# Performance work log

Hardware: AMD Instinct MI355X
Metric: run time of the kernel (lower is better)

Reference implementation:

```python
import jax, jax.numpy as jnp
import numpy as np

B, NQ, NKV = 8, 2048, 2048
DQ, DKV, H = 1024, 1024, 256


def setup_inputs() -> dict:
    key = jax.random.key(0)
    ks = jax.random.split(key, 12)
    s = 0.02
    return {
        "x_q": jax.random.normal(ks[0], (B, NQ, DQ), jnp.float32),
        "x_kv": jax.random.normal(ks[1], (B, NKV, DKV), jnp.float32),
        "bias": jax.random.normal(ks[2], (B, NQ, NKV), jnp.float32),
        "wq_w": jax.random.normal(ks[3], (DQ, H), jnp.float32) * s,
        "wq_b": jnp.zeros((H,), jnp.float32),
        "wk_w": jax.random.normal(ks[4], (DKV, H), jnp.float32) * s,
        "wk_b": jnp.zeros((H,), jnp.float32),
        "wv_w": jax.random.normal(ks[5], (DKV, H), jnp.float32) * s,
        "wv_b": jnp.zeros((H,), jnp.float32),
        "f2_w": jax.random.normal(ks[6], (H, H), jnp.float32) * s,
        "f2_b": jnp.zeros((H,), jnp.float32),
    }


def reference(x_q, x_kv, bias, wq_w, wq_b, wk_w, wk_b, wv_w, wv_b, f2_w, f2_b):
    # Projections: [B, nq, H], [B, nkv, H]
    Q = jnp.einsum('bsd,dh->bsh', x_q, wq_w) + wq_b
    K = jnp.einsum('btd,dh->bth', x_kv, wk_w) + wk_b
    V = jnp.einsum('btd,dh->bth', x_kv, wv_w) + wv_b
    exp_w = jnp.exp(bias)          # [B, nq, nkv]
    exp_K = jnp.exp(K)             # [B, nkv, H]
    num = jnp.einsum('bst,bth->bsh', exp_w, exp_K * V)
    den = jnp.einsum('bst,bth->bsh', exp_w, exp_K)
    Yt = jax.nn.sigmoid(Q) * (num / den)
    return jnp.einsum('bsh,hg->bsg', Yt, f2_w) + f2_b
```

## Files before the change

kernel.cpp:

```cpp
#include <hip/hip_runtime.h>
#include <cstddef>
#include <cstdint>

#define BATCH 8
#define NQ    2048
#define NKV   2048
#define DIN   1024
#define HD    256

typedef __attribute__((ext_vector_type(8))) short bf16x8;
typedef __attribute__((ext_vector_type(4))) float f32x4;

__device__ __forceinline__ float sigmoidf_(float x) {
    return 1.0f / (1.0f + expf(-x));
}

__device__ __forceinline__ unsigned short f2bf(float f) {
    union { float f; unsigned int u; } v;
    v.f = f;
    unsigned int u = v.u;
    return (unsigned short)((u + 0x7FFFu + ((u >> 16) & 1u)) >> 16);
}

#define GLL16(gp, lp)                                                        \
    __builtin_amdgcn_global_load_lds(                                        \
        (const __attribute__((address_space(1))) void*)(gp),                 \
        (__attribute__((address_space(3))) void*)(lp), 16, 0, 0)

__global__ __launch_bounds__(256)
void wtrans_kernel(const float* __restrict__ w0, const float* __restrict__ w1,
                   const float* __restrict__ w2,
                   unsigned short* __restrict__ t0, unsigned short* __restrict__ t1,
                   unsigned short* __restrict__ t2)
{
    const float* w = (blockIdx.z == 0) ? w0 : (blockIdx.z == 1) ? w1 : w2;
    unsigned short* t = (blockIdx.z == 0) ? t0 : (blockIdx.z == 1) ? t1 : t2;
    const int k0 = blockIdx.y * 64;
    const int n0 = blockIdx.x * 64;
    const int tid = threadIdx.x;
    const int kq = tid >> 4;
    const int nq = tid & 15;
    float4 r[4];
#pragma unroll
    for (int i = 0; i < 4; ++i)
        r[i] = *(const float4*)&w[(size_t)(k0 + kq * 4 + i) * HD + n0 + nq * 4];
#pragma unroll
    for (int j = 0; j < 4; ++j) {
        ushort4 o;
        o.x = f2bf(((const float*)&r[0])[j]);
        o.y = f2bf(((const float*)&r[1])[j]);
        o.z = f2bf(((const float*)&r[2])[j]);
        o.w = f2bf(((const float*)&r[3])[j]);
        *(ushort4*)&t[(size_t)(n0 + nq * 4 + j) * DIN + k0 + kq * 4] = o;
    }
}

#define TS 64
#define TH 256
#define TK 32
#define A_LD 40

__global__ __launch_bounds__(256, 1)
void proj_q_mfma(const float* __restrict__ X,
                 const unsigned short* __restrict__ WT,
                 const float* __restrict__ bv,
                 float* __restrict__ sigQ)
{
    __shared__ unsigned short As[2][TS][A_LD];
    __shared__ unsigned short Bs[2][TH * TK];

    const int m0 = blockIdx.x * TS;
    const int tid = threadIdx.x;
    const int lane = tid & 63, wave = tid >> 6;
    const int quad = lane >> 4, l16 = lane & 15;

    const int a_row = tid >> 2, a_koff = (tid & 3) * 8;
    const float* aP = X + (size_t)(m0 + a_row) * DIN + a_koff;

    const unsigned short* bP[4];
    int ldsOff[4];
#pragma unroll
    for (int j = 0; j < 4; ++j) {
        int idx = j * 256 + tid;
        int row = idx >> 2, c = idx & 3;
        int kc = c ^ ((row >> 1) & 3);
        bP[j] = WT + (size_t)row * DIN + kc * 8;
        ldsOff[j] = (j * 256 + wave * 64) * 16;
    }

    f32x4 acc[4][4] = {};
    float4 a0 = *(const float4*)aP;
    float4 a1 = *(const float4*)(aP + 4);

    for (int k0 = 0; k0 < DIN; k0 += TK) {
        const int p = (k0 >> 5) & 1;
        ushort4 q0, q1;
        q0.x = f2bf(a0.x); q0.y = f2bf(a0.y); q0.z = f2bf(a0.z); q0.w = f2bf(a0.w);
        q1.x = f2bf(a1.x); q1.y = f2bf(a1.y); q1.z = f2bf(a1.z); q1.w = f2bf(a1.w);
        *(ushort4*)&As[p][a_row][a_koff]     = q0;
        *(ushort4*)&As[p][a_row][a_koff + 4] = q1;
        char* bL = (char*)&Bs[p][0];
#pragma unroll
        for (int j = 0; j < 4; ++j)
            GLL16(bP[j] + k0, bL + ldsOff[j]);
        __syncthreads();
        if (k0 + TK < DIN) {
            a0 = *(const float4*)(aP + k0 + TK);
            a1 = *(const float4*)(aP + k0 + TK + 4);
        }
        bf16x8 af[4], bf[4];
#pragma unroll
        for (int rt = 0; rt < 4; ++rt)
            af[rt] = *(const bf16x8*)&As[p][rt * 16 + l16][quad * 8];
#pragma unroll
        for (int ct = 0; ct < 4; ++ct) {
            int row = wave * 64 + ct * 16 + l16;
            int off = row * 64 + ((quad ^ ((row >> 1) & 3)) * 16);
            bf[ct] = *(const bf16x8*)((const char*)&Bs[p][0] + off);
        }
#pragma unroll
        for (int rt = 0; rt < 4; ++rt)
#pragma unroll
            for (int ct = 0; ct < 4; ++ct)
                acc[rt][ct] = __builtin_amdgcn_mfma_f32_16x16x32_bf16(
                    af[rt], bf[ct], acc[rt][ct], 0, 0, 0);
        __syncthreads();
    }

#pragma unroll
    for (int rt = 0; rt < 4; ++rt)
#pragma unroll
        for (int ct = 0; ct < 4; ++ct) {
            const int h = wave * 64 + ct * 16 + l16;
            const float bb = bv[h];
#pragma unroll
            for (int r = 0; r < 4; ++r) {
                const int m = m0 + rt * 16 + quad * 4 + r;
                sigQ[(size_t)m * HD + h] = sigmoidf_(acc[rt][ct][r] + bb);
            }
        }
}

__global__ __launch_bounds__(256, 1)
void proj_kv_mfma(const float* __restrict__ X,
                  const unsigned short* __restrict__ WKT,
                  const float* __restrict__ bk,
                  const unsigned short* __restrict__ WVT,
                  const float* __restrict__ bvv,
                  unsigned short* __restrict__ eKt,
                  unsigned short* __restrict__ eKVt)
{
    __shared__ unsigned short As[2][TS][A_LD];
    __shared__ unsigned short Bk[2][TH * TK];
    __shared__ unsigned short Bv[2][TH * TK];

    const int m0 = blockIdx.x * TS;
    const int tid = threadIdx.x;
    const int lane = tid & 63, wave = tid >> 6;
    const int quad = lane >> 4, l16 = lane & 15;

    const int a_row = tid >> 2, a_koff = (tid & 3) * 8;
    const float* aP = X + (size_t)(m0 + a_row) * DIN + a_koff;

    const unsigned short* bkP[4];
    const unsigned short* bvP[4];
    int ldsOff[4];
#pragma unroll
    for (int j = 0; j < 4; ++j) {
        int idx = j * 256 + tid;
        int row = idx >> 2, c = idx & 3;
        int kc = c ^ ((row >> 1) & 3);
        bkP[j] = WKT + (size_t)row * DIN + kc * 8;
        bvP[j] = WVT + (size_t)row * DIN + kc * 8;
        ldsOff[j] = (j * 256 + wave * 64) * 16;
    }

    f32x4 acck[4][4] = {};
    f32x4 accv[4][4] = {};
    float4 a0 = *(const float4*)aP;
    float4 a1 = *(const float4*)(aP + 4);

    for (int k0 = 0; k0 < DIN; k0 += TK) {
        const int p = (k0 >> 5) & 1;
        ushort4 q0, q1;
        q0.x = f2bf(a0.x); q0.y = f2bf(a0.y); q0.z = f2bf(a0.z); q0.w = f2bf(a0.w);
        q1.x = f2bf(a1.x); q1.y = f2bf(a1.y); q1.z = f2bf(a1.z); q1.w = f2bf(a1.w);
        *(ushort4*)&As[p][a_row][a_koff]     = q0;
        *(ushort4*)&As[p][a_row][a_koff + 4] = q1;
        char* bkL = (char*)&Bk[p][0];
        char* bvL = (char*)&Bv[p][0];
#pragma unroll
        for (int j = 0; j < 4; ++j) {
            GLL16(bkP[j] + k0, bkL + ldsOff[j]);
            GLL16(bvP[j] + k0, bvL + ldsOff[j]);
        }
        __syncthreads();
        if (k0 + TK < DIN) {
            a0 = *(const float4*)(aP + k0 + TK);
            a1 = *(const float4*)(aP + k0 + TK + 4);
        }
        bf16x8 af[4], bkf[4], bvf[4];
#pragma unroll
        for (int rt = 0; rt < 4; ++rt)
            af[rt] = *(const bf16x8*)&As[p][rt * 16 + l16][quad * 8];
#pragma unroll
        for (int ct = 0; ct < 4; ++ct) {
            int row = wave * 64 + ct * 16 + l16;
            int off = row * 64 + ((quad ^ ((row >> 1) & 3)) * 16);
            bkf[ct] = *(const bf16x8*)((const char*)&Bk[p][0] + off);
            bvf[ct] = *(const bf16x8*)((const char*)&Bv[p][0] + off);
        }
#pragma unroll
        for (int rt = 0; rt < 4; ++rt)
#pragma unroll
            for (int ct = 0; ct < 4; ++ct) {
                acck[rt][ct] = __builtin_amdgcn_mfma_f32_16x16x32_bf16(
                    af[rt], bkf[ct], acck[rt][ct], 0, 0, 0);
                accv[rt][ct] = __builtin_amdgcn_mfma_f32_16x16x32_bf16(
                    af[rt], bvf[ct], accv[rt][ct], 0, 0, 0);
            }
        __syncthreads();
    }

    const int bidx = m0 >> 11;
    const int tb = m0 & (NKV - 1);
#pragma unroll
    for (int rt = 0; rt < 4; ++rt)
#pragma unroll
        for (int ct = 0; ct < 4; ++ct) {
            const int h = wave * 64 + ct * 16 + l16;
            const float bkb = bk[h];
            const float bvb = bvv[h];
            ushort4 pk, pv;
            unsigned short* pK = (unsigned short*)&pk;
            unsigned short* pV = (unsigned short*)&pv;
#pragma unroll
            for (int r = 0; r < 4; ++r) {
                float e  = __expf(acck[rt][ct][r] + bkb);
                float ev = e * (accv[rt][ct][r] + bvb);
                pK[r] = f2bf(e);
                pV[r] = f2bf(ev);
            }
            const int t0 = tb + rt * 16 + quad * 4;
            size_t base = ((size_t)bidx * HD + h) * NKV + t0;
            *(ushort4*)&eKt[base]  = pk;
            *(ushort4*)&eKVt[base] = pv;
        }
}

__global__ __launch_bounds__(256, 1)
void aft_mfma_kernel(const float* __restrict__ bias,
                     const unsigned short* __restrict__ eKt,
                     const unsigned short* __restrict__ eKVt,
                     const float* __restrict__ sigQ,
                     float* __restrict__ Yt)
{
    __shared__ unsigned short As[2][TS][A_LD];
    __shared__ unsigned short Bn[2][TH * TK];
    __shared__ unsigned short Bd[2][TH * TK];

    const int b  = blockIdx.y;
    const int s0 = blockIdx.x * TS;
    const int tid = threadIdx.x;
    const int lane = tid & 63, wave = tid >> 6;
    const int quad = lane >> 4, l16 = lane & 15;

    const int a_row = tid >> 2, a_koff = (tid & 3) * 8;
    const float* aP = bias + ((size_t)b * NQ + (s0 + a_row)) * NKV + a_koff;

    const unsigned short* bnP[4];
    const unsigned short* bdP[4];
    int ldsOff[4];
#pragma unroll
    for (int j = 0; j < 4; ++j) {
        int idx = j * 256 + tid;
        int row = idx >> 2, c = idx & 3;
        int kc = c ^ ((row >> 1) & 3);
        bnP[j] = eKVt + ((size_t)b * HD + row) * NKV + kc * 8;
        bdP[j] = eKt  + ((size_t)b * HD + row) * NKV + kc * 8;
        ldsOff[j] = (j * 256 + wave * 64) * 16;
    }

    f32x4 accn[4][4] = {};
    f32x4 accd[4][4] = {};
    float4 a0 = *(const float4*)aP;
    float4 a1 = *(const float4*)(aP + 4);

    for (int k0 = 0; k0 < NKV; k0 += TK) {
        const int p = (k0 >> 5) & 1;
        ushort4 q0, q1;
        q0.x = f2bf(__expf(a0.x)); q0.y = f2bf(__expf(a0.y));
        q0.z = f2bf(__expf(a0.z)); q0.w = f2bf(__expf(a0.w));
        q1.x = f2bf(__expf(a1.x)); q1.y = f2bf(__expf(a1.y));
        q1.z = f2bf(__expf(a1.z)); q1.w = f2bf(__expf(a1.w));
        *(ushort4*)&As[p][a_row][a_koff]     = q0;
        *(ushort4*)&As[p][a_row][a_koff + 4] = q1;
        char* bnL = (char*)&Bn[p][0];
        char* bdL = (char*)&Bd[p][0];
#pragma unroll
        for (int j = 0; j < 4; ++j) {
            GLL16(bnP[j] + k0, bnL + ldsOff[j]);
            GLL16(bdP[j] + k0, bdL + ldsOff[j]);
        }
        __syncthreads();
        if (k0 + TK < NKV) {
            a0 = *(const float4*)(aP + k0 + TK);
            a1 = *(const float4*)(aP + k0 + TK + 4);
        }
        bf16x8 af[4], bnf[4], bdf[4];
#pragma unroll
        for (int rt = 0; rt < 4; ++rt)
            af[rt] = *(const bf16x8*)&As[p][rt * 16 + l16][quad * 8];
#pragma unroll
        for (int ct = 0; ct < 4; ++ct) {
            int row = wave * 64 + ct * 16 + l16;
            int off = row * 64 + ((quad ^ ((row >> 1) & 3)) * 16);
            bnf[ct] = *(const bf16x8*)((const char*)&Bn[p][0] + off);
            bdf[ct] = *(const bf16x8*)((const char*)&Bd[p][0] + off);
        }
#pragma unroll
        for (int rt = 0; rt < 4; ++rt)
#pragma unroll
            for (int ct = 0; ct < 4; ++ct) {
                accn[rt][ct] = __builtin_amdgcn_mfma_f32_16x16x32_bf16(
                    af[rt], bnf[ct], accn[rt][ct], 0, 0, 0);
                accd[rt][ct] = __builtin_amdgcn_mfma_f32_16x16x32_bf16(
                    af[rt], bdf[ct], accd[rt][ct], 0, 0, 0);
            }
        __syncthreads();
    }

#pragma unroll
    for (int rt = 0; rt < 4; ++rt)
#pragma unroll
        for (int ct = 0; ct < 4; ++ct) {
            const int h = wave * 64 + ct * 16 + l16;
#pragma unroll
            for (int r = 0; r < 4; ++r) {
                const int s = s0 + rt * 16 + quad * 4 + r;
                const size_t idx = ((size_t)b * NQ + s) * HD + h;
                Yt[idx] = sigQ[idx] * accn[rt][ct][r] / accd[rt][ct][r];
            }
        }
}

#define BM 64
#define BN 64
#define BK 16
#define PADF 4
#define LDAF (BM + PADF)
#define LDBF (BN + PADF)

__global__ __launch_bounds__(256)
void gemm_bias_kernel(const float* __restrict__ X, const float* __restrict__ W,
                      const float* __restrict__ bv, float* __restrict__ out,
                      int M, int N, int K)
{
    __shared__ float As[BK][LDAF];
    __shared__ float Ws[BK][LDBF];
    const int tid = threadIdx.x;
    const int tx = tid & 15, ty = tid >> 4;
    const int row0 = blockIdx.y * BM;
    const int col0 = blockIdx.x * BN;
    const int la_row = tid >> 2, la_col = (tid & 3) * 4;
    const int lw_row = tid >> 4, lw_col = (tid & 15) * 4;

    float acc[4][4] = {};

    const float* Xp = X + (size_t)(row0 + la_row) * K + la_col;
    const float* Wp = W + (size_t)lw_row * N + col0 + lw_col;

    for (int k0 = 0; k0 < K; k0 += BK) {
        float4 av = *(const float4*)(Xp + k0);
        float4 wv = *(const float4*)(Wp + (size_t)k0 * N);
        As[la_col + 0][la_row] = av.x;
        As[la_col + 1][la_row] = av.y;
        As[la_col + 2][la_row] = av.z;
        As[la_col + 3][la_row] = av.w;
        *(float4*)&Ws[lw_row][lw_col] = wv;
        __syncthreads();
#pragma unroll
        for (int kk = 0; kk < BK; ++kk) {
            float4 a4 = *(const float4*)&As[kk][ty * 4];
            float4 w4 = *(const float4*)&Ws[kk][tx * 4];
            float aa[4] = {a4.x, a4.y, a4.z, a4.w};
            float ww[4] = {w4.x, w4.y, w4.z, w4.w};
#pragma unroll
            for (int i = 0; i < 4; ++i)
#pragma unroll
                for (int j = 0; j < 4; ++j)
                    acc[i][j] = fmaf(aa[i], ww[j], acc[i][j]);
        }
        __syncthreads();
    }

    float bb[4];
#pragma unroll
    for (int j = 0; j < 4; ++j) bb[j] = bv[col0 + tx * 4 + j];
#pragma unroll
    for (int i = 0; i < 4; ++i) {
        int r = row0 + ty * 4 + i;
        float4 o;
        o.x = acc[i][0] + bb[0];
        o.y = acc[i][1] + bb[1];
        o.z = acc[i][2] + bb[2];
        o.w = acc[i][3] + bb[3];
        *(float4*)&out[(size_t)r * N + col0 + tx * 4] = o;
    }
}

extern "C" void kernel_launch(void* const* d_in, const int* in_sizes, int n_in,
                              void* d_out, int out_size, void* d_ws, size_t ws_size,
                              hipStream_t stream)
{
    const float* x_q  = (const float*)d_in[0];
    const float* x_kv = (const float*)d_in[1];
    const float* bias = (const float*)d_in[2];
    const float* wq_w = (const float*)d_in[3];
    const float* wq_b = (const float*)d_in[4];
    const float* wk_w = (const float*)d_in[5];
    const float* wk_b = (const float*)d_in[6];
    const float* wv_w = (const float*)d_in[7];
    const float* wv_b = (const float*)d_in[8];
    const float* f2_w = (const float*)d_in[9];
    const float* f2_b = (const float*)d_in[10];
    float* out = (float*)d_out;

    float* ws = (float*)d_ws;
    const size_t nBH = (size_t)BATCH * NQ * HD;
    float* sigQ = ws;
    float* Yt   = ws + nBH;
    unsigned short* eKt  = (unsigned short*)(ws + 2 * nBH);
    unsigned short* eKVt = eKt + nBH;
    unsigned short* wqT  = eKVt + nBH;
    unsigned short* wkT  = wqT + (size_t)HD * DIN;
    unsigned short* wvT  = wkT + (size_t)HD * DIN;

    const int M = BATCH * NQ;
    dim3 blk(256);

    wtrans_kernel<<<dim3(HD / 64, DIN / 64, 3), blk, 0, stream>>>(
        wq_w, wk_w, wv_w, wqT, wkT, wvT);

    proj_q_mfma<<<dim3(M / TS), blk, 0, stream>>>(x_q, wqT, wq_b, sigQ);

    proj_kv_mfma<<<dim3(M / TS), blk, 0, stream>>>(
        x_kv, wkT, wk_b, wvT, wv_b, eKt, eKVt);

    aft_mfma_kernel<<<dim3(NQ / TS, BATCH), blk, 0, stream>>>(
        bias, eKt, eKVt, sigQ, Yt);

    gemm_bias_kernel<<<dim3(HD / BN, M / BM), blk, 0, stream>>>(
        Yt, f2_w, f2_b, out, M, HD, HD);
}
```

Baseline: 429.5 us.

## Halve row tile to 32 and allow two blocks per CU in MFMA kernels

Shrinks the row tile from 64 to 32 rows in the Q, KV and AFT MFMA kernels, remaps the A-tile load so each thread loads one float4, and raises launch bounds to two blocks per CU. The AFT kernel also interleaves batches in its block index so neighbouring blocks share the same query tile position across batches. The aim is more waves per CU and more blocks to fill the GPU, which can hide latency. The cost is that the K/V weight tiles are reloaded twice as often per output row and each block does fewer MFMAs per barrier.

```diff
diff --git a/kernel.cpp b/kernel.cpp
--- a/kernel.cpp
+++ b/kernel.cpp
@@ -55,12 +55,12 @@
     }
 }
 
-#define TS 64
+#define TS 32
 #define TH 256
 #define TK 32
 #define A_LD 40
 
-__global__ __launch_bounds__(256, 1)
+__global__ __launch_bounds__(256, 2)
 void proj_q_mfma(const float* __restrict__ X,
                  const unsigned short* __restrict__ WT,
                  const float* __restrict__ bv,
@@ -74,7 +74,7 @@
     const int lane = tid & 63, wave = tid >> 6;
     const int quad = lane >> 4, l16 = lane & 15;
 
-    const int a_row = tid >> 2, a_koff = (tid & 3) * 8;
+    const int a_row = tid >> 3, a_koff = (tid & 7) * 4;
     const float* aP = X + (size_t)(m0 + a_row) * DIN + a_koff;
 
     const unsigned short* bP[4];
@@ -88,29 +88,24 @@
         ldsOff[j] = (j * 256 + wave * 64) * 16;
     }
 
-    f32x4 acc[4][4] = {};
+    f32x4 acc[2][4] = {};
     float4 a0 = *(const float4*)aP;
-    float4 a1 = *(const float4*)(aP + 4);
 
     for (int k0 = 0; k0 < DIN; k0 += TK) {
         const int p = (k0 >> 5) & 1;
-        ushort4 q0, q1;
+        ushort4 q0;
         q0.x = f2bf(a0.x); q0.y = f2bf(a0.y); q0.z = f2bf(a0.z); q0.w = f2bf(a0.w);
-        q1.x = f2bf(a1.x); q1.y = f2bf(a1.y); q1.z = f2bf(a1.z); q1.w = f2bf(a1.w);
-        *(ushort4*)&As[p][a_row][a_koff]     = q0;
-        *(ushort4*)&As[p][a_row][a_koff + 4] = q1;
+        *(ushort4*)&As[p][a_row][a_koff] = q0;
         char* bL = (char*)&Bs[p][0];
 #pragma unroll
         for (int j = 0; j < 4; ++j)
             GLL16(bP[j] + k0, bL + ldsOff[j]);
         __syncthreads();
-        if (k0 + TK < DIN) {
+        if (k0 + TK < DIN)
             a0 = *(const float4*)(aP + k0 + TK);
-            a1 = *(const float4*)(aP + k0 + TK + 4);
-        }
-        bf16x8 af[4], bf[4];
-#pragma unroll
-        for (int rt = 0; rt < 4; ++rt)
+        bf16x8 af[2], bf[4];
+#pragma unroll
+        for (int rt = 0; rt < 2; ++rt)
             af[rt] = *(const bf16x8*)&As[p][rt * 16 + l16][quad * 8];
 #pragma unroll
         for (int ct = 0; ct < 4; ++ct) {
@@ -119,7 +114,7 @@
             bf[ct] = *(const bf16x8*)((const char*)&Bs[p][0] + off);
         }
 #pragma unroll
-        for (int rt = 0; rt < 4; ++rt)
+        for (int rt = 0; rt < 2; ++rt)
 #pragma unroll
             for (int ct = 0; ct < 4; ++ct)
                 acc[rt][ct] = __builtin_amdgcn_mfma_f32_16x16x32_bf16(
@@ -128,7 +123,7 @@
     }
 
 #pragma unroll
-    for (int rt = 0; rt < 4; ++rt)
+    for (int rt = 0; rt < 2; ++rt)
 #pragma unroll
         for (int ct = 0; ct < 4; ++ct) {
             const int h = wave * 64 + ct * 16 + l16;
@@ -141,7 +136,7 @@
         }
 }
 
-__global__ __launch_bounds__(256, 1)
+__global__ __launch_bounds__(256, 2)
 void proj_kv_mfma(const float* __restrict__ X,
                   const unsigned short* __restrict__ WKT,
                   const float* __restrict__ bk,
@@ -159,7 +154,7 @@
     const int lane = tid & 63, wave = tid >> 6;
     const int quad = lane >> 4, l16 = lane & 15;
 
-    const int a_row = tid >> 2, a_koff = (tid & 3) * 8;
+    const int a_row = tid >> 3, a_koff = (tid & 7) * 4;
     const float* aP = X + (size_t)(m0 + a_row) * DIN + a_koff;
 
     const unsigned short* bkP[4];
@@ -175,18 +170,15 @@
         ldsOff[j] = (j * 256 + wave * 64) * 16;
     }
 
-    f32x4 acck[4][4] = {};
-    f32x4 accv[4][4] = {};
+    f32x4 acck[2][4] = {};
+    f32x4 accv[2][4] = {};
     float4 a0 = *(const float4*)aP;
-    float4 a1 = *(const float4*)(aP + 4);
 
     for (int k0 = 0; k0 < DIN; k0 += TK) {
         const int p = (k0 >> 5) & 1;
-        ushort4 q0, q1;
+        ushort4 q0;
         q0.x = f2bf(a0.x); q0.y = f2bf(a0.y); q0.z = f2bf(a0.z); q0.w = f2bf(a0.w);
-        q1.x = f2bf(a1.x); q1.y = f2bf(a1.y); q1.z = f2bf(a1.z); q1.w = f2bf(a1.w);
-        *(ushort4*)&As[p][a_row][a_koff]     = q0;
-        *(ushort4*)&As[p][a_row][a_koff + 4] = q1;
+        *(ushort4*)&As[p][a_row][a_koff] = q0;
         char* bkL = (char*)&Bk[p][0];
         char* bvL = (char*)&Bv[p][0];
 #pragma unroll
@@ -195,13 +187,11 @@
             GLL16(bvP[j] + k0, bvL + ldsOff[j]);
         }
         __syncthreads();
-        if (k0 + TK < DIN) {
+        if (k0 + TK < DIN)
             a0 = *(const float4*)(aP + k0 + TK);
-            a1 = *(const float4*)(aP + k0 + TK + 4);
-        }
-        bf16x8 af[4], bkf[4], bvf[4];
-#pragma unroll
-        for (int rt = 0; rt < 4; ++rt)
+        bf16x8 af[2], bkf[4], bvf[4];
+#pragma unroll
+        for (int rt = 0; rt < 2; ++rt)
             af[rt] = *(const bf16x8*)&As[p][rt * 16 + l16][quad * 8];
 #pragma unroll
         for (int ct = 0; ct < 4; ++ct) {
@@ -211,7 +201,7 @@
             bvf[ct] = *(const bf16x8*)((const char*)&Bv[p][0] + off);
         }
 #pragma unroll
-        for (int rt = 0; rt < 4; ++rt)
+        for (int rt = 0; rt < 2; ++rt)
 #pragma unroll
             for (int ct = 0; ct < 4; ++ct) {
                 acck[rt][ct] = __builtin_amdgcn_mfma_f32_16x16x32_bf16(
@@ -225,7 +215,7 @@
     const int bidx = m0 >> 11;
     const int tb = m0 & (NKV - 1);
 #pragma unroll
-    for (int rt = 0; rt < 4; ++rt)
+    for (int rt = 0; rt < 2; ++rt)
 #pragma unroll
         for (int ct = 0; ct < 4; ++ct) {
             const int h = wave * 64 + ct * 16 + l16;
@@ -248,7 +238,7 @@
         }
 }
 
-__global__ __launch_bounds__(256, 1)
+__global__ __launch_bounds__(256, 2)
 void aft_mfma_kernel(const float* __restrict__ bias,
                      const unsigned short* __restrict__ eKt,
                      const unsigned short* __restrict__ eKVt,
@@ -259,13 +249,14 @@
     __shared__ unsigned short Bn[2][TH * TK];
     __shared__ unsigned short Bd[2][TH * TK];
 
-    const int b  = blockIdx.y;
-    const int s0 = blockIdx.x * TS;
+    const int lin = blockIdx.y * gridDim.x + blockIdx.x;
+    const int b   = lin & 7;
+    const int s0  = (lin >> 3) * TS;
     const int tid = threadIdx.x;
     const int lane = tid & 63, wave = tid >> 6;
     const int quad = lane >> 4, l16 = lane & 15;
 
-    const int a_row = tid >> 2, a_koff = (tid & 3) * 8;
+    const int a_row = tid >> 3, a_koff = (tid & 7) * 4;
     const float* aP = bias + ((size_t)b * NQ + (s0 + a_row)) * NKV + a_koff;
 
     const unsigned short* bnP[4];
@@ -281,20 +272,16 @@
         ldsOff[j] = (j * 256 + wave * 64) * 16;
     }
 
-    f32x4 accn[4][4] = {};
-    f32x4 accd[4][4] = {};
+    f32x4 accn[2][4] = {};
+    f32x4 accd[2][4] = {};
     float4 a0 = *(const float4*)aP;
-    float4 a1 = *(const float4*)(aP + 4);
 
     for (int k0 = 0; k0 < NKV; k0 += TK) {
         const int p = (k0 >> 5) & 1;
-        ushort4 q0, q1;
+        ushort4 q0;
         q0.x = f2bf(__expf(a0.x)); q0.y = f2bf(__expf(a0.y));
         q0.z = f2bf(__expf(a0.z)); q0.w = f2bf(__expf(a0.w));
-        q1.x = f2bf(__expf(a1.x)); q1.y = f2bf(__expf(a1.y));
-        q1.z = f2bf(__expf(a1.z)); q1.w = f2bf(__expf(a1.w));
-        *(ushort4*)&As[p][a_row][a_koff]     = q0;
-        *(ushort4*)&As[p][a_row][a_koff + 4] = q1;
+        *(ushort4*)&As[p][a_row][a_koff] = q0;
         char* bnL = (char*)&Bn[p][0];
         char* bdL = (char*)&Bd[p][0];
 #pragma unroll
@@ -303,13 +290,11 @@
             GLL16(bdP[j] + k0, bdL + ldsOff[j]);
         }
         __syncthreads();
-        if (k0 + TK < NKV) {
+        if (k0 + TK < NKV)
             a0 = *(const float4*)(aP + k0 + TK);
-            a1 = *(const float4*)(aP + k0 + TK + 4);
-        }
-        bf16x8 af[4], bnf[4], bdf[4];
-#pragma unroll
-        for (int rt = 0; rt < 4; ++rt)
+        bf16x8 af[2], bnf[4], bdf[4];
+#pragma unroll
+        for (int rt = 0; rt < 2; ++rt)
             af[rt] = *(const bf16x8*)&As[p][rt * 16 + l16][quad * 8];
 #pragma unroll
         for (int ct = 0; ct < 4; ++ct) {
@@ -319,7 +304,7 @@
             bdf[ct] = *(const bf16x8*)((const char*)&Bd[p][0] + off);
         }
 #pragma unroll
-        for (int rt = 0; rt < 4; ++rt)
+        for (int rt = 0; rt < 2; ++rt)
 #pragma unroll
             for (int ct = 0; ct < 4; ++ct) {
                 accn[rt][ct] = __builtin_amdgcn_mfma_f32_16x16x32_bf16(
@@ -331,7 +316,7 @@
     }
 
 #pragma unroll
-    for (int rt = 0; rt < 4; ++rt)
+    for (int rt = 0; rt < 2; ++rt)
 #pragma unroll
         for (int ct = 0; ct < 4; ++ct) {
             const int h = wave * 64 + ct * 16 + l16;
```

Measured after the change: 463.3 us. 1.08x slower.

## Software-pipeline MFMA GEMM loops with prefetch and manual waitcnt barriers

Applied to the files above, without the earlier changes.

The three MFMA GEMM kernels now issue the LDS-direct loads for the next B tile, and the fp32 A-operand loads two steps ahead, before the current tile is computed. Explicit s_waitcnt and s_barrier replace __syncthreads so that global memory latency overlaps with MFMA work. The attention-like kernel also remaps block indices so consecutive blocks cycle through batches, and the fp32 output GEMM gains register prefetch of the next tile. The manual vmcnt counts depend on the exact order in which loads are issued. Redundant loads at the tail are clamped to a valid address, adding some extra traffic.

```diff
diff --git a/kernel.cpp b/kernel.cpp
--- a/kernel.cpp
+++ b/kernel.cpp
@@ -26,6 +26,13 @@
     __builtin_amdgcn_global_load_lds(                                        \
         (const __attribute__((address_space(1))) void*)(gp),                 \
         (__attribute__((address_space(3))) void*)(lp), 16, 0, 0)
+
+__device__ __forceinline__ f32x4 gload4(const float* p) {
+    f32x4 r;
+    asm volatile("global_load_dwordx4 %0, %1, off"
+                 : "=v"(r) : "v"(p) : "memory");
+    return r;
+}
 
 __global__ __launch_bounds__(256)
 void wtrans_kernel(const float* __restrict__ w0, const float* __restrict__ w1,
@@ -89,25 +96,32 @@
     }
 
     f32x4 acc[4][4] = {};
-    float4 a0 = *(const float4*)aP;
-    float4 a1 = *(const float4*)(aP + 4);
+
+#pragma unroll
+    for (int j = 0; j < 4; ++j)
+        GLL16(bP[j], (char*)&Bs[0][0] + ldsOff[j]);
+    f32x4 c0 = gload4(aP);
+    f32x4 c1 = gload4(aP + 4);
+    f32x4 n0 = gload4(aP + TK);
+    f32x4 n1 = gload4(aP + TK + 4);
 
     for (int k0 = 0; k0 < DIN; k0 += TK) {
-        const int p = (k0 >> 5) & 1;
+        const int p = (k0 >> 5) & 1, pn = p ^ 1;
+        const int kb = (k0 + TK < DIN) ? (k0 + TK) : (DIN - TK);
+        const int km = (k0 + 2 * TK < DIN) ? (k0 + 2 * TK) : (DIN - TK);
+        char* bL = (char*)&Bs[pn][0];
+#pragma unroll
+        for (int j = 0; j < 4; ++j)
+            GLL16(bP[j] + kb, bL + ldsOff[j]);
+        asm volatile("s_waitcnt vmcnt(4)" : "+v"(c0), "+v"(c1) :: "memory");
         ushort4 q0, q1;
-        q0.x = f2bf(a0.x); q0.y = f2bf(a0.y); q0.z = f2bf(a0.z); q0.w = f2bf(a0.w);
-        q1.x = f2bf(a1.x); q1.y = f2bf(a1.y); q1.z = f2bf(a1.z); q1.w = f2bf(a1.w);
+        q0.x = f2bf(c0[0]); q0.y = f2bf(c0[1]); q0.z = f2bf(c0[2]); q0.w = f2bf(c0[3]);
+        q1.x = f2bf(c1[0]); q1.y = f2bf(c1[1]); q1.z = f2bf(c1[2]); q1.w = f2bf(c1[3]);
         *(ushort4*)&As[p][a_row][a_koff]     = q0;
         *(ushort4*)&As[p][a_row][a_koff + 4] = q1;
-        char* bL = (char*)&Bs[p][0];
-#pragma unroll
-        for (int j = 0; j < 4; ++j)
-            GLL16(bP[j] + k0, bL + ldsOff[j]);
-        __syncthreads();
-        if (k0 + TK < DIN) {
-            a0 = *(const float4*)(aP + k0 + TK);
-            a1 = *(const float4*)(aP + k0 + TK + 4);
-        }
+        f32x4 m0v = gload4(aP + km);
+        f32x4 m1v = gload4(aP + km + 4);
+        asm volatile("s_waitcnt lgkmcnt(0)\ns_barrier" ::: "memory");
         bf16x8 af[4], bf[4];
 #pragma unroll
         for (int rt = 0; rt < 4; ++rt)
@@ -124,7 +138,8 @@
             for (int ct = 0; ct < 4; ++ct)
                 acc[rt][ct] = __builtin_amdgcn_mfma_f32_16x16x32_bf16(
                     af[rt], bf[ct], acc[rt][ct], 0, 0, 0);
-        __syncthreads();
+        asm volatile("s_barrier" ::: "memory");
+        c0 = n0; c1 = n1; n0 = m0v; n1 = m1v;
     }
 
 #pragma unroll
@@ -177,28 +192,37 @@
 
     f32x4 acck[4][4] = {};
     f32x4 accv[4][4] = {};
-    float4 a0 = *(const float4*)aP;
-    float4 a1 = *(const float4*)(aP + 4);
+
+#pragma unroll
+    for (int j = 0; j < 4; ++j) {
+        GLL16(bkP[j], (char*)&Bk[0][0] + ldsOff[j]);
+        GLL16(bvP[j], (char*)&Bv[0][0] + ldsOff[j]);
+    }
+    f32x4 c0 = gload4(aP);
+    f32x4 c1 = gload4(aP + 4);
+    f32x4 n0 = gload4(aP + TK);
+    f32x4 n1 = gload4(aP + TK + 4);
 
     for (int k0 = 0; k0 < DIN; k0 += TK) {
-        const int p = (k0 >> 5) & 1;
+        const int p = (k0 >> 5) & 1, pn = p ^ 1;
+        const int kb = (k0 + TK < DIN) ? (k0 + TK) : (DIN - TK);
+        const int km = (k0 + 2 * TK < DIN) ? (k0 + 2 * TK) : (DIN - TK);
+        char* bkL = (char*)&Bk[pn][0];
+        char* bvL = (char*)&Bv[pn][0];
+#pragma unroll
+        for (int j = 0; j < 4; ++j) {
+            GLL16(bkP[j] + kb, bkL + ldsOff[j]);
+            GLL16(bvP[j] + kb, bvL + ldsOff[j]);
+        }
+        asm volatile("s_waitcnt vmcnt(8)" : "+v"(c0), "+v"(c1) :: "memory");
         ushort4 q0, q1;
-        q0.x = f2bf(a0.x); q0.y = f2bf(a0.y); q0.z = f2bf(a0.z); q0.w = f2bf(a0.w);
-        q1.x = f2bf(a1.x); q1.y = f2bf(a1.y); q1.z = f2bf(a1.z); q1.w = f2bf(a1.w);
+        q0.x = f2bf(c0[0]); q0.y = f2bf(c0[1]); q0.z = f2bf(c0[2]); q0.w = f2bf(c0[3]);
+        q1.x = f2bf(c1[0]); q1.y = f2bf(c1[1]); q1.z = f2bf(c1[2]); q1.w = f2bf(c1[3]);
         *(ushort4*)&As[p][a_row][a_koff]     = q0;
         *(ushort4*)&As[p][a_row][a_koff + 4] = q1;
-        char* bkL = (char*)&Bk[p][0];
-        char* bvL = (char*)&Bv[p][0];
-#pragma unroll
-        for (int j = 0; j < 4; ++j) {
-            GLL16(bkP[j] + k0, bkL + ldsOff[j]);
-            GLL16(bvP[j] + k0, bvL + ldsOff[j]);
-        }
-        __syncthreads();
-        if (k0 + TK < DIN) {
-            a0 = *(const float4*)(aP + k0 + TK);
-            a1 = *(const float4*)(aP + k0 + TK + 4);
-        }
+        f32x4 m0v = gload4(aP + km);
+        f32x4 m1v = gload4(aP + km + 4);
+        asm volatile("s_waitcnt lgkmcnt(0)\ns_barrier" ::: "memory");
         bf16x8 af[4], bkf[4], bvf[4];
 #pragma unroll
         for (int rt = 0; rt < 4; ++rt)
@@ -219,7 +243,8 @@
                 accv[rt][ct] = __builtin_amdgcn_mfma_f32_16x16x32_bf16(
                     af[rt], bvf[ct], accv[rt][ct], 0, 0, 0);
             }
-        __syncthreads();
+        asm volatile("s_barrier" ::: "memory");
+        c0 = n0; c1 = n1; n0 = m0v; n1 = m1v;
     }
 
     const int bidx = m0 >> 11;
@@ -259,8 +284,9 @@
     __shared__ unsigned short Bn[2][TH * TK];
     __shared__ unsigned short Bd[2][TH * TK];
 
-    const int b  = blockIdx.y;
-    const int s0 = blockIdx.x * TS;
+    const int lin = blockIdx.y * gridDim.x + blockIdx.x;
+    const int b   = lin & 7;
+    const int s0  = (lin >> 3) * TS;
     const int tid = threadIdx.x;
     const int lane = tid & 63, wave = tid >> 6;
     const int quad = lane >> 4, l16 = lane & 15;
@@ -283,30 +309,39 @@
 
     f32x4 accn[4][4] = {};
     f32x4 accd[4][4] = {};
-    float4 a0 = *(const float4*)aP;
-    float4 a1 = *(const float4*)(aP + 4);
+
+#pragma unroll
+    for (int j = 0; j < 4; ++j) {
+        GLL16(bnP[j], (char*)&Bn[0][0] + ldsOff[j]);
+        GLL16(bdP[j], (char*)&Bd[0][0] + ldsOff[j]);
+    }
+    f32x4 c0 = gload4(aP);
+    f32x4 c1 = gload4(aP + 4);
+    f32x4 n0 = gload4(aP + TK);
+    f32x4 n1 = gload4(aP + TK + 4);
 
     for (int k0 = 0; k0 < NKV; k0 += TK) {
-        const int p = (k0 >> 5) & 1;
+        const int p = (k0 >> 5) & 1, pn = p ^ 1;
+        const int kb = (k0 + TK < NKV) ? (k0 + TK) : (NKV - TK);
+        const int km = (k0 + 2 * TK < NKV) ? (k0 + 2 * TK) : (NKV - TK);
+        char* bnL = (char*)&Bn[pn][0];
+        char* bdL = (char*)&Bd[pn][0];
+#pragma unroll
+        for (int j = 0; j < 4; ++j) {
+            GLL16(bnP[j] + kb, bnL + ldsOff[j]);
+            GLL16(bdP[j] + kb, bdL + ldsOff[j]);
+        }
+        asm volatile("s_waitcnt vmcnt(8)" : "+v"(c0), "+v"(c1) :: "memory");
         ushort4 q0, q1;
-        q0.x = f2bf(__expf(a0.x)); q0.y = f2bf(__expf(a0.y));
-        q0.z = f2bf(__expf(a0.z)); q0.w = f2bf(__expf(a0.w));
-        q1.x = f2bf(__expf(a1.x)); q1.y = f2bf(__expf(a1.y));
-        q1.z = f2bf(__expf(a1.z)); q1.w = f2bf(__expf(a1.w));
+        q0.x = f2bf(__expf(c0[0])); q0.y = f2bf(__expf(c0[1]));
+        q0.z = f2bf(__expf(c0[2])); q0.w = f2bf(__expf(c0[3]));
+        q1.x = f2bf(__expf(c1[0])); q1.y = f2bf(__expf(c1[1]));
+        q1.z = f2bf(__expf(c1[2])); q1.w = f2bf(__expf(c1[3]));
         *(ushort4*)&As[p][a_row][a_koff]     = q0;
         *(ushort4*)&As[p][a_row][a_koff + 4] = q1;
-        char* bnL = (char*)&Bn[p][0];
-        char* bdL = (char*)&Bd[p][0];
-#pragma unroll
-        for (int j = 0; j < 4; ++j) {
-            GLL16(bnP[j] + k0, bnL + ldsOff[j]);
-            GLL16(bdP[j] + k0, bdL + ldsOff[j]);
-        }
-        __syncthreads();
-        if (k0 + TK < NKV) {
-            a0 = *(const float4*)(aP + k0 + TK);
-            a1 = *(const float4*)(aP + k0 + TK + 4);
-        }
+        f32x4 m0v = gload4(aP + km);
+        f32x4 m1v = gload4(aP + km + 4);
+        asm volatile("s_waitcnt lgkmcnt(0)\ns_barrier" ::: "memory");
         bf16x8 af[4], bnf[4], bdf[4];
 #pragma unroll
         for (int rt = 0; rt < 4; ++rt)
@@ -327,7 +362,8 @@
                 accd[rt][ct] = __builtin_amdgcn_mfma_f32_16x16x32_bf16(
                     af[rt], bdf[ct], accd[rt][ct], 0, 0, 0);
             }
-        __syncthreads();
+        asm volatile("s_barrier" ::: "memory");
+        c0 = n0; c1 = n1; n0 = m0v; n1 = m1v;
     }
 
 #pragma unroll
@@ -370,15 +406,20 @@
     const float* Xp = X + (size_t)(row0 + la_row) * K + la_col;
     const float* Wp = W + (size_t)lw_row * N + col0 + lw_col;
 
+    float4 av = *(const float4*)Xp;
+    float4 wv = *(const float4*)Wp;
+
     for (int k0 = 0; k0 < K; k0 += BK) {
-        float4 av = *(const float4*)(Xp + k0);
-        float4 wv = *(const float4*)(Wp + (size_t)k0 * N);
         As[la_col + 0][la_row] = av.x;
         As[la_col + 1][la_row] = av.y;
         As[la_col + 2][la_row] = av.z;
         As[la_col + 3][la_row] = av.w;
         *(float4*)&Ws[lw_row][lw_col] = wv;
         __syncthreads();
+        if (k0 + BK < K) {
+            av = *(const float4*)(Xp + k0 + BK);
+            wv = *(const float4*)(Wp + (size_t)(k0 + BK) * N);
+        }
 #pragma unroll
         for (int kk = 0; kk < BK; ++kk) {
             float4 a4 = *(const float4*)&As[kk][ty * 4];
```

Result: slower. 456.7 us (+6.4%).

## Pre-tile B operands into swizzled k-tile layout, single-buffer LDS, raise occupancy

Applied to the files above, without the earlier changes.

Weight transposes and the exp(K)/exp(K)V producers now write B operands directly in a k-tile-contiguous, pre-swizzled layout, so each 32-wide k slab is one contiguous 16KB chunk read with coalesced global_load_lds. LDS double buffers are dropped to single buffers and launch bounds raised to allow 2-3 blocks per CU, trading intra-block overlap for inter-block occupancy. The AFT kernel remaps block indices so consecutive blocks span different batches, and the fp32 output GEMM prefetches the next tile into registers. Single buffering risks exposing load latency if occupancy gains do not materialise.

```diff
diff --git a/kernel.cpp b/kernel.cpp
--- a/kernel.cpp
+++ b/kernel.cpp
@@ -26,6 +26,7 @@
     __builtin_amdgcn_global_load_lds(                                        \
         (const __attribute__((address_space(1))) void*)(gp),                 \
         (__attribute__((address_space(3))) void*)(lp), 16, 0, 0)
+
 
 __global__ __launch_bounds__(256)
 void wtrans_kernel(const float* __restrict__ w0, const float* __restrict__ w1,
@@ -44,14 +45,19 @@
 #pragma unroll
     for (int i = 0; i < 4; ++i)
         r[i] = *(const float4*)&w[(size_t)(k0 + kq * 4 + i) * HD + n0 + nq * 4];
+    const int k = k0 + kq * 4;
+    const int kt = k >> 5;
+    const int c  = (k & 31) >> 3;
 #pragma unroll
     for (int j = 0; j < 4; ++j) {
+        const int h = n0 + nq * 4 + j;
         ushort4 o;
         o.x = f2bf(((const float*)&r[0])[j]);
         o.y = f2bf(((const float*)&r[1])[j]);
         o.z = f2bf(((const float*)&r[2])[j]);
         o.w = f2bf(((const float*)&r[3])[j]);
-        *(ushort4*)&t[(size_t)(n0 + nq * 4 + j) * DIN + k0 + kq * 4] = o;
+        const int kc = c ^ ((h >> 1) & 3);
+        *(ushort4*)&t[((size_t)kt * 256 + h) * 32 + kc * 8 + (k & 7)] = o;
     }
 }
 
@@ -60,14 +66,14 @@
 #define TK 32
 #define A_LD 40
 
-__global__ __launch_bounds__(256, 1)
+__global__ __launch_bounds__(256, 3)
 void proj_q_mfma(const float* __restrict__ X,
                  const unsigned short* __restrict__ WT,
                  const float* __restrict__ bv,
                  float* __restrict__ sigQ)
 {
-    __shared__ unsigned short As[2][TS][A_LD];
-    __shared__ unsigned short Bs[2][TH * TK];
+    __shared__ unsigned short As[TS][A_LD];
+    __shared__ unsigned short Bs[TH * TK];
 
     const int m0 = blockIdx.x * TS;
     const int tid = threadIdx.x;
@@ -81,10 +87,7 @@
     int ldsOff[4];
 #pragma unroll
     for (int j = 0; j < 4; ++j) {
-        int idx = j * 256 + tid;
-        int row = idx >> 2, c = idx & 3;
-        int kc = c ^ ((row >> 1) & 3);
-        bP[j] = WT + (size_t)row * DIN + kc * 8;
+        bP[j] = WT + ((size_t)j * 256 + tid) * 8;
         ldsOff[j] = (j * 256 + wave * 64) * 16;
     }
 
@@ -93,16 +96,15 @@
     float4 a1 = *(const float4*)(aP + 4);
 
     for (int k0 = 0; k0 < DIN; k0 += TK) {
-        const int p = (k0 >> 5) & 1;
         ushort4 q0, q1;
         q0.x = f2bf(a0.x); q0.y = f2bf(a0.y); q0.z = f2bf(a0.z); q0.w = f2bf(a0.w);
         q1.x = f2bf(a1.x); q1.y = f2bf(a1.y); q1.z = f2bf(a1.z); q1.w = f2bf(a1.w);
-        *(ushort4*)&As[p][a_row][a_koff]     = q0;
-        *(ushort4*)&As[p][a_row][a_koff + 4] = q1;
-        char* bL = (char*)&Bs[p][0];
+        *(ushort4*)&As[a_row][a_koff]     = q0;
+        *(ushort4*)&As[a_row][a_koff + 4] = q1;
+        char* bL = (char*)&Bs[0];
 #pragma unroll
         for (int j = 0; j < 4; ++j)
-            GLL16(bP[j] + k0, bL + ldsOff[j]);
+            GLL16(bP[j] + (size_t)k0 * 256, bL + ldsOff[j]);
         __syncthreads();
         if (k0 + TK < DIN) {
             a0 = *(const float4*)(aP + k0 + TK);
@@ -111,12 +113,12 @@
         bf16x8 af[4], bf[4];
 #pragma unroll
         for (int rt = 0; rt < 4; ++rt)
-            af[rt] = *(const bf16x8*)&As[p][rt * 16 + l16][quad * 8];
+            af[rt] = *(const bf16x8*)&As[rt * 16 + l16][quad * 8];
 #pragma unroll
         for (int ct = 0; ct < 4; ++ct) {
             int row = wave * 64 + ct * 16 + l16;
             int off = row * 64 + ((quad ^ ((row >> 1) & 3)) * 16);
-            bf[ct] = *(const bf16x8*)((const char*)&Bs[p][0] + off);
+            bf[ct] = *(const bf16x8*)((const char*)&Bs[0] + off);
         }
 #pragma unroll
         for (int rt = 0; rt < 4; ++rt)
@@ -141,7 +143,7 @@
         }
 }
 
-__global__ __launch_bounds__(256, 1)
+__global__ __launch_bounds__(256, 2)
 void proj_kv_mfma(const float* __restrict__ X,
                   const unsigned short* __restrict__ WKT,
                   const float* __restrict__ bk,
@@ -150,9 +152,9 @@
                   unsigned short* __restrict__ eKt,
                   unsigned short* __restrict__ eKVt)
 {
-    __shared__ unsigned short As[2][TS][A_LD];
-    __shared__ unsigned short Bk[2][TH * TK];
-    __shared__ unsigned short Bv[2][TH * TK];
+    __shared__ unsigned short As[TS][A_LD];
+    __shared__ unsigned short Bk[TH * TK];
+    __shared__ unsigned short Bv[TH * TK];
 
     const int m0 = blockIdx.x * TS;
     const int tid = threadIdx.x;
@@ -167,11 +169,8 @@
     int ldsOff[4];
 #pragma unroll
     for (int j = 0; j < 4; ++j) {
-        int idx = j * 256 + tid;
-        int row = idx >> 2, c = idx & 3;
-        int kc = c ^ ((row >> 1) & 3);
-        bkP[j] = WKT + (size_t)row * DIN + kc * 8;
-        bvP[j] = WVT + (size_t)row * DIN + kc * 8;
+        bkP[j] = WKT + ((size_t)j * 256 + tid) * 8;
+        bvP[j] = WVT + ((size_t)j * 256 + tid) * 8;
         ldsOff[j] = (j * 256 + wave * 64) * 16;
     }
 
@@ -181,18 +180,17 @@
     float4 a1 = *(const float4*)(aP + 4);
 
     for (int k0 = 0; k0 < DIN; k0 += TK) {
-        const int p = (k0 >> 5) & 1;
         ushort4 q0, q1;
         q0.x = f2bf(a0.x); q0.y = f2bf(a0.y); q0.z = f2bf(a0.z); q0.w = f2bf(a0.w);
         q1.x = f2bf(a1.x); q1.y = f2bf(a1.y); q1.z = f2bf(a1.z); q1.w = f2bf(a1.w);
-        *(ushort4*)&As[p][a_row][a_koff]     = q0;
-        *(ushort4*)&As[p][a_row][a_koff + 4] = q1;
-        char* bkL = (char*)&Bk[p][0];
-        char* bvL = (char*)&Bv[p][0];
+        *(ushort4*)&As[a_row][a_koff]     = q0;
+        *(ushort4*)&As[a_row][a_koff + 4] = q1;
+        char* bkL = (char*)&Bk[0];
+        char* bvL = (char*)&Bv[0];
 #pragma unroll
         for (int j = 0; j < 4; ++j) {
-            GLL16(bkP[j] + k0, bkL + ldsOff[j]);
-            GLL16(bvP[j] + k0, bvL + ldsOff[j]);
+            GLL16(bkP[j] + (size_t)k0 * 256, bkL + ldsOff[j]);
+            GLL16(bvP[j] + (size_t)k0 * 256, bvL + ldsOff[j]);
         }
         __syncthreads();
         if (k0 + TK < DIN) {
@@ -202,13 +200,13 @@
         bf16x8 af[4], bkf[4], bvf[4];
 #pragma unroll
         for (int rt = 0; rt < 4; ++rt)
-            af[rt] = *(const bf16x8*)&As[p][rt * 16 + l16][quad * 8];
+            af[rt] = *(const bf16x8*)&As[rt * 16 + l16][quad * 8];
 #pragma unroll
         for (int ct = 0; ct < 4; ++ct) {
             int row = wave * 64 + ct * 16 + l16;
             int off = row * 64 + ((quad ^ ((row >> 1) & 3)) * 16);
-            bkf[ct] = *(const bf16x8*)((const char*)&Bk[p][0] + off);
-            bvf[ct] = *(const bf16x8*)((const char*)&Bv[p][0] + off);
+            bkf[ct] = *(const bf16x8*)((const char*)&Bk[0] + off);
+            bvf[ct] = *(const bf16x8*)((const char*)&Bv[0] + off);
         }
 #pragma unroll
         for (int rt = 0; rt < 4; ++rt)
@@ -241,26 +239,30 @@
                 pK[r] = f2bf(e);
                 pV[r] = f2bf(ev);
             }
-            const int t0 = tb + rt * 16 + quad * 4;
-            size_t base = ((size_t)bidx * HD + h) * NKV + t0;
-            *(ushort4*)&eKt[base]  = pk;
-            *(ushort4*)&eKVt[base] = pv;
-        }
-}
-
-__global__ __launch_bounds__(256, 1)
+            const int t0a = tb + rt * 16 + quad * 4;
+            const int tt = t0a >> 5, tc = t0a & 31;
+            const int kc = (tc >> 3) ^ ((h >> 1) & 3);
+            size_t idx = (((size_t)bidx * (NKV / 32) + tt) * 256 + h) * 32
+                         + kc * 8 + (tc & 7);
+            *(ushort4*)&eKt[idx]  = pk;
+            *(ushort4*)&eKVt[idx] = pv;
+        }
+}
+
+__global__ __launch_bounds__(256, 2)
 void aft_mfma_kernel(const float* __restrict__ bias,
                      const unsigned short* __restrict__ eKt,
                      const unsigned short* __restrict__ eKVt,
                      const float* __restrict__ sigQ,
                      float* __restrict__ Yt)
 {
-    __shared__ unsigned short As[2][TS][A_LD];
-    __shared__ unsigned short Bn[2][TH * TK];
-    __shared__ unsigned short Bd[2][TH * TK];
-
-    const int b  = blockIdx.y;
-    const int s0 = blockIdx.x * TS;
+    __shared__ unsigned short As[TS][A_LD];
+    __shared__ unsigned short Bn[TH * TK];
+    __shared__ unsigned short Bd[TH * TK];
+
+    const int lin = blockIdx.y * gridDim.x + blockIdx.x;
+    const int b   = lin & 7;
+    const int s0  = (lin >> 3) * TS;
     const int tid = threadIdx.x;
     const int lane = tid & 63, wave = tid >> 6;
     const int quad = lane >> 4, l16 = lane & 15;
@@ -273,11 +275,9 @@
     int ldsOff[4];
 #pragma unroll
     for (int j = 0; j < 4; ++j) {
-        int idx = j * 256 + tid;
-        int row = idx >> 2, c = idx & 3;
-        int kc = c ^ ((row >> 1) & 3);
-        bnP[j] = eKVt + ((size_t)b * HD + row) * NKV + kc * 8;
-        bdP[j] = eKt  + ((size_t)b * HD + row) * NKV + kc * 8;
+        const size_t base = (size_t)b * (NKV / 32) * 256 * 32;
+        bnP[j] = eKVt + base + ((size_t)j * 256 + tid) * 8;
+        bdP[j] = eKt  + base + ((size_t)j * 256 + tid) * 8;
         ldsOff[j] = (j * 256 + wave * 64) * 16;
     }
 
@@ -287,20 +287,19 @@
     float4 a1 = *(const float4*)(aP + 4);
 
     for (int k0 = 0; k0 < NKV; k0 += TK) {
-        const int p = (k0 >> 5) & 1;
         ushort4 q0, q1;
         q0.x = f2bf(__expf(a0.x)); q0.y = f2bf(__expf(a0.y));
         q0.z = f2bf(__expf(a0.z)); q0.w = f2bf(__expf(a0.w));
         q1.x = f2bf(__expf(a1.x)); q1.y = f2bf(__expf(a1.y));
         q1.z = f2bf(__expf(a1.z)); q1.w = f2bf(__expf(a1.w));
-        *(ushort4*)&As[p][a_row][a_koff]     = q0;
-        *(ushort4*)&As[p][a_row][a_koff + 4] = q1;
-        char* bnL = (char*)&Bn[p][0];
-        char* bdL = (char*)&Bd[p][0];
+        *(ushort4*)&As[a_row][a_koff]     = q0;
+        *(ushort4*)&As[a_row][a_koff + 4] = q1;
+        char* bnL = (char*)&Bn[0];
+        char* bdL = (char*)&Bd[0];
 #pragma unroll
         for (int j = 0; j < 4; ++j) {
-            GLL16(bnP[j] + k0, bnL + ldsOff[j]);
-            GLL16(bdP[j] + k0, bdL + ldsOff[j]);
+            GLL16(bnP[j] + (size_t)k0 * 256, bnL + ldsOff[j]);
+            GLL16(bdP[j] + (size_t)k0 * 256, bdL + ldsOff[j]);
         }
         __syncthreads();
         if (k0 + TK < NKV) {
@@ -310,13 +309,13 @@
         bf16x8 af[4], bnf[4], bdf[4];
 #pragma unroll
         for (int rt = 0; rt < 4; ++rt)
-            af[rt] = *(const bf16x8*)&As[p][rt * 16 + l16][quad * 8];
+            af[rt] = *(const bf16x8*)&As[rt * 16 + l16][quad * 8];
 #pragma unroll
         for (int ct = 0; ct < 4; ++ct) {
             int row = wave * 64 + ct * 16 + l16;
             int off = row * 64 + ((quad ^ ((row >> 1) & 3)) * 16);
-            bnf[ct] = *(const bf16x8*)((const char*)&Bn[p][0] + off);
-            bdf[ct] = *(const bf16x8*)((const char*)&Bd[p][0] + off);
+            bnf[ct] = *(const bf16x8*)((const char*)&Bn[0] + off);
+            bdf[ct] = *(const bf16x8*)((const char*)&Bd[0] + off);
         }
 #pragma unroll
         for (int rt = 0; rt < 4; ++rt)
@@ -370,15 +369,20 @@
     const float* Xp = X + (size_t)(row0 + la_row) * K + la_col;
     const float* Wp = W + (size_t)lw_row * N + col0 + lw_col;
 
+    float4 av = *(const float4*)Xp;
+    float4 wv = *(const float4*)Wp;
+
     for (int k0 = 0; k0 < K; k0 += BK) {
-        float4 av = *(const float4*)(Xp + k0);
-        float4 wv = *(const float4*)(Wp + (size_t)k0 * N);
         As[la_col + 0][la_row] = av.x;
         As[la_col + 1][la_row] = av.y;
         As[la_col + 2][la_row] = av.z;
         As[la_col + 3][la_row] = av.w;
         *(float4*)&Ws[lw_row][lw_col] = wv;
         __syncthreads();
+        if (k0 + BK < K) {
+            av = *(const float4*)(Xp + k0 + BK);
+            wv = *(const float4*)(Wp + (size_t)(k0 + BK) * N);
+        }
 #pragma unroll
         for (int kk = 0; kk < BK; ++kk) {
             float4 a4 = *(const float4*)&As[kk][ty * 4];
```

Result: slower. 441.9 us (+2.9%).
